# Optimization experiments

Hardware: AMD Instinct MI355X
Metric: run time of the kernel (lower is better)

The kernel has to match this reference:

```python
import jax, jax.numpy as jnp
import numpy as np

N, E, NG = 4096, 8192, 256
AF, BF, H, L = 9, 4, 128, 3
LN_EPS = 1e-5


def _layernorm(x, g, b):
    mu = jnp.mean(x, axis=-1, keepdims=True)
    var = jnp.var(x, axis=-1, keepdims=True)
    return (x - mu) * jax.lax.rsqrt(var + LN_EPS) * g + b


def setup_inputs() -> dict:
    key = jax.random.key(0)
    ks = jax.random.split(key, 20)
    x = jax.random.normal(ks[0], (N, AF), dtype=jnp.float32)
    edge_index = jax.random.randint(ks[1], (2, E), 0, N, dtype=jnp.int64)
    edge_attr = jax.random.normal(ks[2], (E, BF), dtype=jnp.float32)
    batch = jnp.sort(jax.random.randint(ks[3], (N,), 0, NG, dtype=jnp.int64))
    s = lambda f: 1.0 / np.sqrt(f)
    return {
        "x": x, "edge_index": edge_index, "edge_attr": edge_attr, "batch": batch,
        "atom_w": jax.random.normal(ks[4], (AF, H), jnp.float32) * s(AF),
        "atom_b": jnp.zeros((H,), jnp.float32),
        # per-layer edge-network params, stacked over L layers
        "e1_w": jax.random.normal(ks[5], (L, BF, H), jnp.float32) * s(BF),
        "e1_b": jnp.zeros((L, H), jnp.float32),
        "e2_w": jax.random.normal(ks[6], (L, H, H * H), jnp.float32) * s(H),
        "e2_b": jnp.zeros((L, H * H), jnp.float32),
        "root_w": jax.random.normal(ks[7], (L, H, H), jnp.float32) * s(H),
        "conv_b": jnp.zeros((L, H), jnp.float32),
        "ln_g": jnp.ones((L, H), jnp.float32),
        "ln_b": jnp.zeros((L, H), jnp.float32),
        "head_w1": jax.random.normal(ks[8], (H, H // 2), jnp.float32) * s(H),
        "head_b1": jnp.zeros((H // 2,), jnp.float32),
        "head_w2": jax.random.normal(ks[9], (H // 2, 1), jnp.float32) * s(H // 2),
        "head_b2": jnp.zeros((1,), jnp.float32),
    }


def reference(x, edge_index, edge_attr, batch, atom_w, atom_b, e1_w, e1_b,
              e2_w, e2_b, root_w, conv_b, ln_g, ln_b, head_w1, head_b1,
              head_w2, head_b2):
    src, dst = edge_index[0], edge_index[1]
    h = jax.nn.relu(x @ atom_w + atom_b)  # [N, H]
    # in-degree for mean aggregation (empty -> 0 via clamp on denominator)
    deg = jax.ops.segment_sum(jnp.ones((E,), h.dtype), dst, num_segments=N)
    denom = jnp.maximum(deg, 1.0)[:, None]
    for l in range(L):
        # edge network: bond features -> per-edge HxH weight matrix
        eh = jax.nn.gelu(edge_attr @ e1_w[l] + e1_b[l], approximate=False)
        w = (eh @ e2_w[l] + e2_b[l]).reshape(E, H, H)  # [E, H, H]
        # gather source node features, per-edge matvec, scatter-mean to dst
        msg = jnp.einsum('ei,eio->eo', h[src], w)  # [E, H]
        agg = jax.ops.segment_sum(msg, dst, num_segments=N) / denom
        h_new = jax.nn.relu(agg + h @ root_w[l] + conv_b[l])
        h = _layernorm(h + h_new, ln_g[l], ln_b[l])
        # dropout: eval mode (identity)
    # global mean pool over graphs
    cnt = jnp.maximum(jax.ops.segment_sum(jnp.ones((N,), h.dtype), batch, num_segments=NG), 1.0)
    mol = jax.ops.segment_sum(h, batch, num_segments=NG) / cnt[:, None]
    hid = jax.nn.gelu(mol @ head_w1 + head_b1, approximate=False)
    logits = (hid @ head_w2 + head_b2).squeeze(-1)  # [NG]
    return logits
```

## Files before the change

kernel.cpp:

```cpp
#include <hip/hip_runtime.h>
#include <hip/hip_bf16.h>

#define N_NODES 4096
#define N_EDGES 8192
#define NGRAPH  256
#define AFEAT   9
#define BFEAT   4
#define H       128
#define NL      3
#define KS      129
#define SPLITS  4
#define TILE_E  64
#define NPB     4
#define SLICE_SH    16384
#define SLICE_BYTES 32768

typedef short short8 __attribute__((ext_vector_type(8)));
typedef float f32x4 __attribute__((ext_vector_type(4)));

__device__ __forceinline__ short f2b(float f){
    union { float f; unsigned u; } c; c.f = f;
    unsigned r = c.u + 0x7FFFu + ((c.u >> 16) & 1u);
    return (short)(r >> 16);
}
__device__ __forceinline__ float gelu_exact(float x){
    return 0.5f * x * (1.0f + erff(x * 0.70710678118654752440f));
}

__global__ void k_prep_b(const float* __restrict__ e2w, const float* __restrict__ e2b,
                         short* __restrict__ bt){
    __shared__ float ts[H][33];
    int b  = blockIdx.x;
    int o0 = (b & 3) * 32;
    int k  = (b >> 2) % KS;
    int l  = (b >> 2) / KS;
    const float* src = (k < H) ? (e2w + ((size_t)l * H + k) * (H * H))
                               : (e2b + (size_t)l * (H * H));
    for (int idx = threadIdx.x; idx < H * 32; idx += 256){
        int i = idx >> 5, op = idx & 31;
        ts[i][op] = src[i * H + o0 + op];
    }
    __syncthreads();
    short* dst = bt + (size_t)(l * KS + k) * SLICE_SH;
    for (int idx = threadIdx.x; idx < 32 * H; idx += 256){
        int j    = idx & 7;
        int quad = (idx >> 3) & 3;
        int op   = (idx >> 5) & 31;
        int ic   = idx >> 10;
        int i    = ic * 32 + quad * 8 + j;
        int o    = o0 + op;
        dst[((((o >> 4) * 4 + ic) * 64) + quad * 16 + (o & 15)) * 8 + j] = f2b(ts[i][op]);
    }
}

__global__ void k_atom(const float* __restrict__ x, const float* __restrict__ aw,
                       const float* __restrict__ ab, float* __restrict__ h,
                       short* __restrict__ hb){
    __shared__ float xs[AFEAT];
    int n = blockIdx.x, o = threadIdx.x;
    if (o < AFEAT) xs[o] = x[n * AFEAT + o];
    __syncthreads();
    float a = ab[o];
    #pragma unroll
    for (int f = 0; f < AFEAT; ++f) a += xs[f] * aw[f * H + o];
    a = fmaxf(a, 0.0f);
    h[(size_t)n * H + o]  = a;
    hb[(size_t)n * H + o] = f2b(a);
}

__global__ void k_deg(const int* __restrict__ ei, int* __restrict__ ideg){
    int e = blockIdx.x * 256 + threadIdx.x;
    if (e < N_EDGES) atomicAdd(&ideg[ei[N_EDGES + e]], 1);
}

__global__ void k_scan(const int* __restrict__ ideg, int* __restrict__ row_ptr,
                       int* __restrict__ cursor){
    __shared__ int part[256];
    int t = threadIdx.x;
    int base = t * 16;
    int loc[16]; int s = 0;
    #pragma unroll
    for (int i = 0; i < 16; ++i){ loc[i] = s; s += ideg[base + i]; }
    part[t] = s;
    __syncthreads();
    if (t == 0){
        int run = 0;
        for (int i = 0; i < 256; ++i){ int v = part[i]; part[i] = run; run += v; }
        row_ptr[N_NODES] = run;
    }
    __syncthreads();
    int off = part[t];
    #pragma unroll
    for (int i = 0; i < 16; ++i){
        row_ptr[base + i] = off + loc[i];
        cursor[base + i]  = off + loc[i];
    }
}

__global__ void k_fill(const int* __restrict__ ei, int* __restrict__ cursor,
                       int* __restrict__ eidx){
    int e = blockIdx.x * 256 + threadIdx.x;
    if (e < N_EDGES){
        int d = ei[N_EDGES + e];
        int pos = atomicAdd(&cursor[d], 1);
        eidx[pos] = e;
    }
}

__global__ void k_edge_mlp(const float* __restrict__ ea, const float* __restrict__ w1,
                           const float* __restrict__ b1, float* __restrict__ ehT){
    int o = blockIdx.x >> 5;
    int e = (blockIdx.x & 31) * 256 + threadIdx.x;
    float4 a = *(const float4*)(ea + (size_t)e * BFEAT);
    #pragma unroll
    for (int l = 0; l < NL; ++l){
        float v = b1[l * H + o]
                + a.x * w1[(l * BFEAT + 0) * H + o]
                + a.y * w1[(l * BFEAT + 1) * H + o]
                + a.z * w1[(l * BFEAT + 2) * H + o]
                + a.w * w1[(l * BFEAT + 3) * H + o];
        v = gelu_exact(v);
        ehT[((size_t)l * KS + o) * N_EDGES + e] = v;
        if (o == 0) ehT[((size_t)l * KS + H) * N_EDGES + e] = 1.0f;
    }
}

__global__ __launch_bounds__(256, 2)
void k_msg_gemm(const short* __restrict__ bt, const float* __restrict__ ehT,
                const short* __restrict__ hb, const int* __restrict__ ei,
                float* __restrict__ parts, int l){
    __shared__ __align__(16) float ehs[33 * TILE_E];

    const int tid  = threadIdx.x;
    const int lane = tid & 63, w = tid >> 6;
    const int col  = lane & 15, quad = lane >> 4;

    const int so    = blockIdx.x & 7;
    const int split = so & 3;
    const int ohalf = so >> 2;
    const int tile  = blockIdx.x >> 3;
    const int t     = ohalf * 4 + w;
    const int kbeg  = (KS * split) >> 2;
    const int kend  = (KS * (split + 1)) >> 2;
    const int kcnt  = kend - kbeg;
    const int ebase = tile * TILE_E;

    for (int idx = tid; idx < kcnt * TILE_E; idx += 256){
        int kk = idx >> 6, e = idx & 63;
        ehs[idx] = ehT[((size_t)(l * KS + kbeg + kk)) * N_EDGES + ebase + e];
    }

    short8 gf[4][4];
    #pragma unroll
    for (int m = 0; m < 4; ++m){
        int e = ebase + m * 16 + col;
        int s = ei[e];
        const char* gb = (const char*)hb + ((size_t)s * H + quad * 8) * 2;
        #pragma unroll
        for (int ic = 0; ic < 4; ++ic)
            gf[m][ic] = *(const short8*)(gb + ic * 64);
    }

    float acc[4][4];
    #pragma unroll
    for (int m = 0; m < 4; ++m)
        #pragma unroll
        for (int r = 0; r < 4; ++r) acc[m][r] = 0.0f;

    const char* bsrc = (const char*)bt + (size_t)(l * KS + kbeg) * SLICE_BYTES
                     + t * 4096 + lane * 16;

    short8 X[4], Y[4], Z[4];

    auto loadB = [&](short8 (&B)[4], int kk){
        const char* p = bsrc + (size_t)kk * SLICE_BYTES;
        #pragma unroll
        for (int ic = 0; ic < 4; ++ic)
            B[ic] = *(const short8*)(p + ic * 1024);
    };
    auto computeB = [&](const short8 (&B)[4], int kk){
        __builtin_amdgcn_s_setprio(1);
        #pragma unroll
        for (int m = 0; m < 4; ++m){
            f32x4 ev = *(const f32x4*)(ehs + kk * TILE_E + m * 16 + quad * 4);
            f32x4 U = {0.0f, 0.0f, 0.0f, 0.0f};
            #pragma unroll
            for (int ic = 0; ic < 4; ++ic)
                U = __builtin_amdgcn_mfma_f32_16x16x32_bf16(gf[m][ic], B[ic], U, 0, 0, 0);
            #pragma unroll
            for (int r = 0; r < 4; ++r)
                acc[m][r] += ev[r] * U[r];
        }
        __builtin_amdgcn_s_setprio(0);
    };

    loadB(X, 0); loadB(Y, 1); loadB(Z, 2);
    __syncthreads();

    int kk = 0;
    for (; kk + 3 < kcnt; kk += 3){
        computeB(X, kk);     loadB(X, kk + 3);
        computeB(Y, kk + 1); if (kk + 4 < kcnt) loadB(Y, kk + 4);
        computeB(Z, kk + 2); if (kk + 5 < kcnt) loadB(Z, kk + 5);
    }
    computeB(X, kk);
    if (kk + 1 < kcnt) computeB(Y, kk + 1);
    if (kk + 2 < kcnt) computeB(Z, kk + 2);

    float* pb = parts + (size_t)split * N_EDGES * H + (size_t)ebase * H + t * 16;
    #pragma unroll
    for (int m = 0; m < 4; ++m)
        #pragma unroll
        for (int r = 0; r < 4; ++r)
            pb[(size_t)(m * 16 + quad * 4 + r) * H + col] = acc[m][r];
}

__global__ void k_node(const float* __restrict__ parts, const int* __restrict__ eidx,
                       const int* __restrict__ row_ptr,
                       const float* __restrict__ rw, const float* __restrict__ cb,
                       const float* __restrict__ lg, const float* __restrict__ lb,
                       float* __restrict__ h, short* __restrict__ hb,
                       const int* __restrict__ batch, float* __restrict__ molsum,
                       float* __restrict__ cnt, int l, int dolast){
    __shared__ float hs[NPB][H];
    __shared__ float red[NPB][2][2];
    int n0 = blockIdx.x * NPB, o = threadIdx.x;
    const float* W = rw + (size_t)l * H * H;

    float hv[NPB], root[NPB], a[NPB];
    #pragma unroll
    for (int m = 0; m < NPB; ++m){
        hv[m] = h[(size_t)(n0 + m) * H + o];
        hs[m][o] = hv[m];
        root[m] = cb[l * H + o];
    }
    __syncthreads();

    #pragma unroll
    for (int m = 0; m < NPB; ++m){
        int p0 = row_ptr[n0 + m], p1 = row_ptr[n0 + m + 1];
        float s = 0.0f;
        for (int p = p0; p < p1; ++p){
            const float* pr = parts + (size_t)eidx[p] * H + o;
            #pragma unroll
            for (int sp = 0; sp < SPLITS; ++sp) s += pr[(size_t)sp * N_EDGES * H];
        }
        int d = p1 - p0;
        a[m] = s / (float)(d > 0 ? d : 1);
    }

    #pragma unroll 8
    for (int i = 0; i < H; ++i){
        float wv = W[i * H + o];
        #pragma unroll
        for (int m = 0; m < NPB; ++m) root[m] += hs[m][i] * wv;
    }

    float v[NPB];
    #pragma unroll
    for (int m = 0; m < NPB; ++m){
        float hn = fmaxf(a[m] + root[m], 0.0f);
        v[m] = hv[m] + hn;
        float s = v[m], q = v[m] * v[m];
        #pragma unroll
        for (int off = 32; off > 0; off >>= 1){
            s += __shfl_down(s, off, 64);
            q += __shfl_down(q, off, 64);
        }
        if ((o & 63) == 0){ red[m][0][o >> 6] = s; red[m][1][o >> 6] = q; }
    }
    __syncthreads();
    #pragma unroll
    for (int m = 0; m < NPB; ++m){
        float S = red[m][0][0] + red[m][0][1];
        float Q = red[m][1][0] + red[m][1][1];
        float mean = S * (1.0f / H);
        float var  = Q * (1.0f / H) - mean * mean;
        float out  = (v[m] - mean) * rsqrtf(var + 1e-5f) * lg[l * H + o] + lb[l * H + o];
        int n = n0 + m;
        h[(size_t)n * H + o]  = out;
        hb[(size_t)n * H + o] = f2b(out);
        if (dolast){
            int b = batch[n];
            atomicAdd(&molsum[b * H + o], out);
            if (o == 0) atomicAdd(&cnt[b], 1.0f);
        }
    }
}

__global__ void k_head(const float* __restrict__ molsum, const float* __restrict__ cnt,
                       const float* __restrict__ w1, const float* __restrict__ b1,
                       const float* __restrict__ w2, const float* __restrict__ b2,
                       float* __restrict__ out){
    __shared__ float mol[H];
    int g = blockIdx.x, t = threadIdx.x;
    float c = fmaxf(cnt[g], 1.0f);
    mol[t]      = molsum[g * H + t] / c;
    mol[t + 64] = molsum[g * H + t + 64] / c;
    __syncthreads();
    float a = b1[t];
    #pragma unroll 8
    for (int i = 0; i < H; ++i) a += mol[i] * w1[i * 64 + t];
    float hid = gelu_exact(a);
    float p = hid * w2[t];
    #pragma unroll
    for (int off = 32; off > 0; off >>= 1) p += __shfl_down(p, off, 64);
    if (t == 0) out[g] = p + b2[0];
}

extern "C" void kernel_launch(void* const* d_in, const int* in_sizes, int n_in,
                              void* d_out, int out_size, void* d_ws, size_t ws_size,
                              hipStream_t stream){
    (void)in_sizes; (void)n_in; (void)out_size; (void)ws_size;
    const float* x     = (const float*)d_in[0];
    const int*   ei    = (const int*)  d_in[1];
    const float* ea    = (const float*)d_in[2];
    const int*   batch = (const int*)  d_in[3];
    const float* aw    = (const float*)d_in[4];
    const float* ab    = (const float*)d_in[5];
    const float* e1w   = (const float*)d_in[6];
    const float* e1b   = (const float*)d_in[7];
    const float* e2w   = (const float*)d_in[8];
    const float* e2b   = (const float*)d_in[9];
    const float* rw    = (const float*)d_in[10];
    const float* cb    = (const float*)d_in[11];
    const float* lg    = (const float*)d_in[12];
    const float* lb    = (const float*)d_in[13];
    const float* hw1   = (const float*)d_in[14];
    const float* hb1   = (const float*)d_in[15];
    const float* hw2   = (const float*)d_in[16];
    const float* hb2   = (const float*)d_in[17];
    float* out = (float*)d_out;

    char* p = (char*)d_ws;
    auto carve = [&](size_t bytes){ char* r = p; p += (bytes + 255) & ~(size_t)255; return r; };
    short* bt     = (short*)carve((size_t)NL * KS * SLICE_SH * 2);
    float* h      = (float*)carve((size_t)N_NODES * H * 4);
    short* hbuf   = (short*)carve((size_t)N_NODES * H * 2);
    float* ehT    = (float*)carve((size_t)NL * KS * N_EDGES * 4);
    float* parts  = (float*)carve((size_t)SPLITS * N_EDGES * H * 4);
    int*   ideg   = (int*)  carve((size_t)N_NODES * 4);
    int*   row_ptr= (int*)  carve((size_t)(N_NODES + 1) * 4);
    int*   cursor = (int*)  carve((size_t)N_NODES * 4);
    int*   eidx   = (int*)  carve((size_t)N_EDGES * 4);
    float* molsum = (float*)carve((size_t)NGRAPH * H * 4);
    float* cnt    = (float*)carve((size_t)NGRAPH * 4);

    hipMemsetAsync(ideg, 0, (size_t)N_NODES * 4, stream);
    hipMemsetAsync(molsum, 0, (size_t)NGRAPH * H * 4, stream);
    hipMemsetAsync(cnt, 0, (size_t)NGRAPH * 4, stream);

    k_prep_b<<<NL * KS * 4, 256, 0, stream>>>(e2w, e2b, bt);
    k_atom<<<N_NODES, H, 0, stream>>>(x, aw, ab, h, hbuf);
    k_deg<<<N_EDGES / 256, 256, 0, stream>>>(ei, ideg);
    k_scan<<<1, 256, 0, stream>>>(ideg, row_ptr, cursor);
    k_fill<<<N_EDGES / 256, 256, 0, stream>>>(ei, cursor, eidx);
    k_edge_mlp<<<H * (N_EDGES / 256), 256, 0, stream>>>(ea, e1w, e1b, ehT);

    for (int l = 0; l < NL; ++l){
        k_msg_gemm<<<(N_EDGES / TILE_E) * 8, 256, 0, stream>>>(bt, ehT, hbuf, ei, parts, l);
        k_node<<<N_NODES / NPB, H, 0, stream>>>(parts, eidx, row_ptr, rw, cb, lg, lb,
                                                h, hbuf, batch, molsum, cnt, l,
                                                l == NL - 1 ? 1 : 0);
    }
    k_head<<<NGRAPH, 64, 0, stream>>>(molsum, cnt, hw1, hb1, hw2, hb2, out);
}
```

Before: 293.5 us.

## Fuse preprocessing kernels, build CSR in one block, interleave split partials

Merges the edge-MLP, atom embedding and B-weight repacking into one launch using block-index ranges. Degree counting, scan and fill are folded into a single-block kernel with a shared-memory histogram, which also zeroes the pooling buffers and so removes three memsets and two launches. The split partial sums are now stored interleaved per edge, so the node kernel reads all four splits of an edge contiguously. The trade-off is that the single-block CSR build serialises work over all edges, and the fused kernel mixes heterogeneous block types.

```diff
diff --git a/kernel.cpp b/kernel.cpp
--- a/kernel.cpp
+++ b/kernel.cpp
@@ -15,6 +15,10 @@
 #define SLICE_SH    16384
 #define SLICE_BYTES 32768
 
+#define EMLP_BLOCKS (H * (N_EDGES / 256))
+#define ATOM_BLOCKS (N_NODES / 2)
+#define PREP_BLOCKS (NL * KS * 4)
+
 typedef short short8 __attribute__((ext_vector_type(8)));
 typedef float f32x4 __attribute__((ext_vector_type(4)));
 
@@ -27,60 +31,86 @@
     return 0.5f * x * (1.0f + erff(x * 0.70710678118654752440f));
 }
 
-__global__ void k_prep_b(const float* __restrict__ e2w, const float* __restrict__ e2b,
-                         short* __restrict__ bt){
-    __shared__ float ts[H][33];
-    int b  = blockIdx.x;
-    int o0 = (b & 3) * 32;
-    int k  = (b >> 2) % KS;
-    int l  = (b >> 2) / KS;
-    const float* src = (k < H) ? (e2w + ((size_t)l * H + k) * (H * H))
-                               : (e2b + (size_t)l * (H * H));
-    for (int idx = threadIdx.x; idx < H * 32; idx += 256){
-        int i = idx >> 5, op = idx & 31;
-        ts[i][op] = src[i * H + o0 + op];
-    }
-    __syncthreads();
-    short* dst = bt + (size_t)(l * KS + k) * SLICE_SH;
-    for (int idx = threadIdx.x; idx < 32 * H; idx += 256){
-        int j    = idx & 7;
-        int quad = (idx >> 3) & 3;
-        int op   = (idx >> 5) & 31;
-        int ic   = idx >> 10;
-        int i    = ic * 32 + quad * 8 + j;
-        int o    = o0 + op;
-        dst[((((o >> 4) * 4 + ic) * 64) + quad * 16 + (o & 15)) * 8 + j] = f2b(ts[i][op]);
-    }
-}
-
-__global__ void k_atom(const float* __restrict__ x, const float* __restrict__ aw,
-                       const float* __restrict__ ab, float* __restrict__ h,
-                       short* __restrict__ hb){
-    __shared__ float xs[AFEAT];
-    int n = blockIdx.x, o = threadIdx.x;
-    if (o < AFEAT) xs[o] = x[n * AFEAT + o];
-    __syncthreads();
-    float a = ab[o];
-    #pragma unroll
-    for (int f = 0; f < AFEAT; ++f) a += xs[f] * aw[f * H + o];
-    a = fmaxf(a, 0.0f);
-    h[(size_t)n * H + o]  = a;
-    hb[(size_t)n * H + o] = f2b(a);
-}
-
-__global__ void k_deg(const int* __restrict__ ei, int* __restrict__ ideg){
-    int e = blockIdx.x * 256 + threadIdx.x;
-    if (e < N_EDGES) atomicAdd(&ideg[ei[N_EDGES + e]], 1);
-}
-
-__global__ void k_scan(const int* __restrict__ ideg, int* __restrict__ row_ptr,
-                       int* __restrict__ cursor){
+__global__ void k_fused_pre(const float* __restrict__ ea, const float* __restrict__ w1,
+                            const float* __restrict__ b1, float* __restrict__ ehT,
+                            const float* __restrict__ x, const float* __restrict__ aw,
+                            const float* __restrict__ ab, float* __restrict__ h,
+                            short* __restrict__ hb,
+                            const float* __restrict__ e2w, const float* __restrict__ e2b,
+                            short* __restrict__ bt){
+    __shared__ float smem[H * 33];
+    int bid = blockIdx.x, tid = threadIdx.x;
+
+    if (bid < EMLP_BLOCKS){
+        int o = bid >> 5;
+        int e = (bid & 31) * 256 + tid;
+        float4 a = *(const float4*)(ea + (size_t)e * BFEAT);
+        #pragma unroll
+        for (int l = 0; l < NL; ++l){
+            float v = b1[l * H + o]
+                    + a.x * w1[(l * BFEAT + 0) * H + o]
+                    + a.y * w1[(l * BFEAT + 1) * H + o]
+                    + a.z * w1[(l * BFEAT + 2) * H + o]
+                    + a.w * w1[(l * BFEAT + 3) * H + o];
+            v = gelu_exact(v);
+            ehT[((size_t)l * KS + o) * N_EDGES + e] = v;
+            if (o == 0) ehT[((size_t)l * KS + H) * N_EDGES + e] = 1.0f;
+        }
+    } else if (bid < EMLP_BLOCKS + ATOM_BLOCKS){
+        int b = bid - EMLP_BLOCKS;
+        int half = tid >> 7, o = tid & 127;
+        int n = b * 2 + half;
+        float* xs = smem + half * 16;
+        if (o < AFEAT) xs[o] = x[n * AFEAT + o];
+        __syncthreads();
+        float a = ab[o];
+        #pragma unroll
+        for (int f = 0; f < AFEAT; ++f) a += xs[f] * aw[f * H + o];
+        a = fmaxf(a, 0.0f);
+        h[(size_t)n * H + o]  = a;
+        hb[(size_t)n * H + o] = f2b(a);
+    } else {
+        int b  = bid - (EMLP_BLOCKS + ATOM_BLOCKS);
+        int o0 = (b & 3) * 32;
+        int k  = (b >> 2) % KS;
+        int l  = (b >> 2) / KS;
+        const float* src = (k < H) ? (e2w + ((size_t)l * H + k) * (H * H))
+                                   : (e2b + (size_t)l * (H * H));
+        for (int idx = tid; idx < H * 32; idx += 256){
+            int i = idx >> 5, op = idx & 31;
+            smem[i * 33 + op] = src[i * H + o0 + op];
+        }
+        __syncthreads();
+        short* dst = bt + (size_t)(l * KS + k) * SLICE_SH;
+        for (int idx = tid; idx < 32 * H; idx += 256){
+            int j    = idx & 7;
+            int quad = (idx >> 3) & 3;
+            int op   = (idx >> 5) & 31;
+            int ic   = idx >> 10;
+            int i    = ic * 32 + quad * 8 + j;
+            int o    = o0 + op;
+            dst[((((o >> 4) * 4 + ic) * 64) + quad * 16 + (o & 15)) * 8 + j]
+                = f2b(smem[i * 33 + op]);
+        }
+    }
+}
+
+__global__ void k_csr(const int* __restrict__ ei, int* __restrict__ row_ptr,
+                      int* __restrict__ eidx, float* __restrict__ molsum,
+                      float* __restrict__ cnt){
+    __shared__ int hist[N_NODES];
     __shared__ int part[256];
     int t = threadIdx.x;
+    for (int i = t; i < N_NODES; i += 256) hist[i] = 0;
+    for (int i = t; i < NGRAPH * H; i += 256) molsum[i] = 0.0f;
+    for (int i = t; i < NGRAPH; i += 256) cnt[i] = 0.0f;
+    __syncthreads();
+    for (int e = t; e < N_EDGES; e += 256) atomicAdd(&hist[ei[N_EDGES + e]], 1);
+    __syncthreads();
     int base = t * 16;
     int loc[16]; int s = 0;
     #pragma unroll
-    for (int i = 0; i < 16; ++i){ loc[i] = s; s += ideg[base + i]; }
+    for (int i = 0; i < 16; ++i){ loc[i] = s; s += hist[base + i]; }
     part[t] = s;
     __syncthreads();
     if (t == 0){
@@ -91,37 +121,15 @@
     __syncthreads();
     int off = part[t];
     #pragma unroll
-    for (int i = 0; i < 16; ++i){
-        row_ptr[base + i] = off + loc[i];
-        cursor[base + i]  = off + loc[i];
-    }
-}
-
-__global__ void k_fill(const int* __restrict__ ei, int* __restrict__ cursor,
-                       int* __restrict__ eidx){
-    int e = blockIdx.x * 256 + threadIdx.x;
-    if (e < N_EDGES){
+    for (int i = 0; i < 16; ++i) row_ptr[base + i] = off + loc[i];
+    __syncthreads();
+    #pragma unroll
+    for (int i = 0; i < 16; ++i) hist[base + i] = off + loc[i];
+    __syncthreads();
+    for (int e = t; e < N_EDGES; e += 256){
         int d = ei[N_EDGES + e];
-        int pos = atomicAdd(&cursor[d], 1);
+        int pos = atomicAdd(&hist[d], 1);
         eidx[pos] = e;
-    }
-}
-
-__global__ void k_edge_mlp(const float* __restrict__ ea, const float* __restrict__ w1,
-                           const float* __restrict__ b1, float* __restrict__ ehT){
-    int o = blockIdx.x >> 5;
-    int e = (blockIdx.x & 31) * 256 + threadIdx.x;
-    float4 a = *(const float4*)(ea + (size_t)e * BFEAT);
-    #pragma unroll
-    for (int l = 0; l < NL; ++l){
-        float v = b1[l * H + o]
-                + a.x * w1[(l * BFEAT + 0) * H + o]
-                + a.y * w1[(l * BFEAT + 1) * H + o]
-                + a.z * w1[(l * BFEAT + 2) * H + o]
-                + a.w * w1[(l * BFEAT + 3) * H + o];
-        v = gelu_exact(v);
-        ehT[((size_t)l * KS + o) * N_EDGES + e] = v;
-        if (o == 0) ehT[((size_t)l * KS + H) * N_EDGES + e] = 1.0f;
     }
 }
 
@@ -207,12 +215,14 @@
     if (kk + 1 < kcnt) computeB(Y, kk + 1);
     if (kk + 2 < kcnt) computeB(Z, kk + 2);
 
-    float* pb = parts + (size_t)split * N_EDGES * H + (size_t)ebase * H + t * 16;
+    float* pb = parts + ((size_t)ebase * SPLITS + split) * H + t * 16;
     #pragma unroll
     for (int m = 0; m < 4; ++m)
         #pragma unroll
-        for (int r = 0; r < 4; ++r)
-            pb[(size_t)(m * 16 + quad * 4 + r) * H + col] = acc[m][r];
+        for (int r = 0; r < 4; ++r){
+            int row = m * 16 + quad * 4 + r;
+            pb[(size_t)row * SPLITS * H + col] = acc[m][r];
+        }
 }
 
 __global__ void k_node(const float* __restrict__ parts, const int* __restrict__ eidx,
@@ -241,9 +251,9 @@
         int p0 = row_ptr[n0 + m], p1 = row_ptr[n0 + m + 1];
         float s = 0.0f;
         for (int p = p0; p < p1; ++p){
-            const float* pr = parts + (size_t)eidx[p] * H + o;
+            const float* pr = parts + (size_t)eidx[p] * SPLITS * H + o;
             #pragma unroll
-            for (int sp = 0; sp < SPLITS; ++sp) s += pr[(size_t)sp * N_EDGES * H];
+            for (int sp = 0; sp < SPLITS; ++sp) s += pr[sp * H];
         }
         int d = p1 - p0;
         a[m] = s / (float)(d > 0 ? d : 1);
@@ -338,24 +348,15 @@
     float* h      = (float*)carve((size_t)N_NODES * H * 4);
     short* hbuf   = (short*)carve((size_t)N_NODES * H * 2);
     float* ehT    = (float*)carve((size_t)NL * KS * N_EDGES * 4);
-    float* parts  = (float*)carve((size_t)SPLITS * N_EDGES * H * 4);
-    int*   ideg   = (int*)  carve((size_t)N_NODES * 4);
+    float* parts  = (float*)carve((size_t)N_EDGES * SPLITS * H * 4);
     int*   row_ptr= (int*)  carve((size_t)(N_NODES + 1) * 4);
-    int*   cursor = (int*)  carve((size_t)N_NODES * 4);
     int*   eidx   = (int*)  carve((size_t)N_EDGES * 4);
     float* molsum = (float*)carve((size_t)NGRAPH * H * 4);
     float* cnt    = (float*)carve((size_t)NGRAPH * 4);
 
-    hipMemsetAsync(ideg, 0, (size_t)N_NODES * 4, stream);
-    hipMemsetAsync(molsum, 0, (size_t)NGRAPH * H * 4, stream);
-    hipMemsetAsync(cnt, 0, (size_t)NGRAPH * 4, stream);
-
-    k_prep_b<<<NL * KS * 4, 256, 0, stream>>>(e2w, e2b, bt);
-    k_atom<<<N_NODES, H, 0, stream>>>(x, aw, ab, h, hbuf);
-    k_deg<<<N_EDGES / 256, 256, 0, stream>>>(ei, ideg);
-    k_scan<<<1, 256, 0, stream>>>(ideg, row_ptr, cursor);
-    k_fill<<<N_EDGES / 256, 256, 0, stream>>>(ei, cursor, eidx);
-    k_edge_mlp<<<H * (N_EDGES / 256), 256, 0, stream>>>(ea, e1w, e1b, ehT);
+    k_fused_pre<<<EMLP_BLOCKS + ATOM_BLOCKS + PREP_BLOCKS, 256, 0, stream>>>(
+        ea, e1w, e1b, ehT, x, aw, ab, h, hbuf, e2w, e2b, bt);
+    k_csr<<<1, 256, 0, stream>>>(ei, row_ptr, eidx, molsum, cnt);
 
     for (int l = 0; l < NL; ++l){
         k_msg_gemm<<<(N_EDGES / TILE_E) * 8, 256, 0, stream>>>(bt, ehT, hbuf, ei, parts, l);
```

Result: no change. 299.1 us (+1.9%).
